# Performance work log

Measured on AMD Instinct MI355X. Metric: run time of the kernel, lower is better.

Reference implementation:

```python
import jax, jax.numpy as jnp
import numpy as np

B, T, S, D, H = 4, 1024, 1024, 1024, 16
DH = D // H  # head dim = 64
EPS = 1e-5
NEG = -1e9  # finite stand-in for -inf (grad-safe)


def setup_inputs() -> dict:
    key = jax.random.key(0)
    ks = jax.random.split(key, 9)
    std = D ** -0.5
    return {
        "q": jax.random.normal(ks[0], (B, T, D), jnp.float32),
        "k": jax.random.normal(ks[1], (B, S, D), jnp.float32),
        "v": jax.random.normal(ks[2], (B, S, D), jnp.float32),
        "attn_mask": jax.random.randint(ks[3], (T, S), 0, 2) == 1,
        "attn_bias": jax.random.normal(ks[4], (H, T, S), jnp.float32) * 0.1,
        "Wq": jax.random.normal(ks[5], (D, D), jnp.float32) * std,
        "Wk": jax.random.normal(ks[6], (D, D), jnp.float32) * std,
        "Wv": jax.random.normal(ks[7], (D, D), jnp.float32) * std,
        "Wo": jax.random.normal(ks[8], (D, D), jnp.float32) * std,
    }


def reference(q, k, v, attn_mask, attn_bias, Wq, Wk, Wv, Wo):
    # project and split heads: [B,T,D] -> [B,H,T,DH]
    qh = (q @ Wq.T).reshape(B, T, H, DH).transpose(0, 2, 1, 3) * (DH ** -0.5)
    kh = (k @ Wk.T).reshape(B, S, H, DH).transpose(0, 2, 1, 3)
    vh = (v @ Wv.T).reshape(B, S, H, DH).transpose(0, 2, 1, 3)
    # scores [B,H,T,S] with bias broadcast over batch, mask over (B,H)
    attn = jnp.einsum('bhtd,bhsd->bhts', qh, kh) + attn_bias
    attn = jnp.where(attn_mask, NEG, attn)
    # inverted softmax: normalize jointly over (heads, target) for each source pos
    a = jax.nn.softmax(attn.reshape(B, H * T, S), axis=1).reshape(B, H, T, S)
    a = jnp.where(attn_mask, 0.0, a)
    a = a / (a.sum(axis=-1, keepdims=True) + EPS)
    out = jnp.einsum('bhts,bhsd->bhtd', a, vh).transpose(0, 2, 1, 3).reshape(B, T, D)
    return out @ Wo.T
```

## Files before the change

kernel.cpp:

```cpp
#include <hip/hip_runtime.h>
#include <hip/hip_bf16.h>
#include <math.h>
#include <stdint.h>

#define B_ 4
#define T_ 1024
#define S_ 1024
#define D_ 1024
#define H_ 16
#define DH_ 64

static constexpr float EPSV = 1e-5f;
static constexpr float LOG2E = 1.4426950408889634f;
static constexpr float NEG2 = -1.4426950e9f;
static constexpr float SCALE_Q = 0.125f * LOG2E;

typedef __attribute__((ext_vector_type(8))) short short8;
typedef __attribute__((ext_vector_type(4))) float f32x4;

#define MFMA_BF16 __builtin_amdgcn_mfma_f32_16x16x32_bf16

__device__ __forceinline__ ushort f2bf(float f) {
  union { float f; unsigned u; } v; v.f = f;
  unsigned r = (v.u + 0x7FFFu + ((v.u >> 16) & 1u)) >> 16;
  return (ushort)r;
}
__device__ __forceinline__ float bf2f(ushort u) {
  union { unsigned u; float f; } v; v.u = (unsigned)u << 16;
  return v.f;
}
__device__ __forceinline__ float exp2_fast(float x) {
  float r;
  asm("v_exp_f32 %0, %1" : "=v"(r) : "v"(x));
  return r;
}
__device__ __forceinline__ unsigned cvt_pk_bf16(float lo, float hi) {
  unsigned r;
  asm("v_cvt_pk_bf16_f32 %0, %1, %2" : "=v"(r) : "v"(lo), "v"(hi));
  return r;
}

__device__ __forceinline__ void gl_lds16(const ushort* g, ushort* l) {
  __builtin_amdgcn_global_load_lds(
      (const __attribute__((address_space(1))) unsigned int*)g,
      (__attribute__((address_space(3))) unsigned int*)l, 16, 0, 0);
}

__global__ __launch_bounds__(256) void k_prep(
    const float* __restrict__ q, const float* __restrict__ k,
    const float* __restrict__ v, const float* __restrict__ Wq,
    const float* __restrict__ Wk, const float* __restrict__ Wv,
    const float* __restrict__ Wo, const float* __restrict__ bias,
    const int* __restrict__ mask, ushort* __restrict__ qb,
    ushort* __restrict__ kb, ushort* __restrict__ vb,
    ushort* __restrict__ Wqb, ushort* __restrict__ Wkb,
    ushort* __restrict__ Wvb, ushort* __restrict__ Wob,
    ushort* __restrict__ bm) {
  const int bid = blockIdx.x;
  if (bid < 12288) {
    const int which = bid >> 12, local = bid & 4095;
    const float* src = (which == 0) ? q : (which == 1) ? k : v;
    ushort* dst = (which == 0) ? qb : (which == 1) ? kb : vb;
    const int i = (local * 256 + threadIdx.x) * 4;
    float4 t = *(const float4*)(src + i);
    *(ushort4*)(dst + i) = make_ushort4(f2bf(t.x), f2bf(t.y), f2bf(t.z), f2bf(t.w));
  } else if (bid < 16384) {
    const int wv_ = bid - 12288;
    const int which = wv_ >> 10, local = wv_ & 1023;
    const float* src = (which == 0) ? Wq : (which == 1) ? Wk : (which == 2) ? Wv : Wo;
    ushort* dst = (which == 0) ? Wqb : (which == 1) ? Wkb : (which == 2) ? Wvb : Wob;
    const int i = (local * 256 + threadIdx.x) * 4;
    float4 t = *(const float4*)(src + i);
    *(ushort4*)(dst + i) = make_ushort4(f2bf(t.x), f2bf(t.y), f2bf(t.z), f2bf(t.w));
  } else {
    const size_t i = ((size_t)(bid - 16384) * 256 + threadIdx.x) * 8;
    const size_t mi = i & (size_t)(T_ * S_ - 1);
    float4 b0 = *(const float4*)(bias + i);
    float4 b1 = *(const float4*)(bias + i + 4);
    int4 m0 = *(const int4*)(mask + mi);
    int4 m1 = *(const int4*)(mask + mi + 4);
    ushort o[8];
    o[0] = f2bf(m0.x ? NEG2 : b0.x * LOG2E); o[1] = f2bf(m0.y ? NEG2 : b0.y * LOG2E);
    o[2] = f2bf(m0.z ? NEG2 : b0.z * LOG2E); o[3] = f2bf(m0.w ? NEG2 : b0.w * LOG2E);
    o[4] = f2bf(m1.x ? NEG2 : b1.x * LOG2E); o[5] = f2bf(m1.y ? NEG2 : b1.y * LOG2E);
    o[6] = f2bf(m1.z ? NEG2 : b1.z * LOG2E); o[7] = f2bf(m1.w ? NEG2 : b1.w * LOG2E);
    *(uint4*)(bm + i) = *(uint4*)o;
  }
}

template <int MODE>
__global__ __launch_bounds__(256) void k_gemm(const ushort* __restrict__ A,
                                              const ushort* __restrict__ W,
                                              void* __restrict__ Yv,
                                              float scale) {
  __shared__ ushort At[128][32];
  __shared__ ushort Wt[128][32];
  const int tid = threadIdx.x;
  const int l = tid & 63, w = tid >> 6;
  const int wm = (w >> 1) * 64, wn = (w & 1) * 64;
  const int r16 = l & 15, g = l >> 4;
  const int i0 = blockIdx.x * 128, j0 = blockIdx.y * 128;
  const int srow = (l >> 2), scol = (l & 3) << 3;
  f32x4 acc[4][4] = {};

  for (int k0 = 0; k0 < D_; k0 += 32) {
    __syncthreads();
#pragma unroll
    for (int u = 0; u < 2; ++u) {
      const int row = w * 32 + u * 16 + srow;
      gl_lds16(&A[(size_t)(i0 + row) * D_ + k0 + scol], &At[w * 32 + u * 16][0]);
      gl_lds16(&W[(size_t)(j0 + row) * D_ + k0 + scol], &Wt[w * 32 + u * 16][0]);
    }
    __syncthreads();
    short8 a0[4], b0[4];
#pragma unroll
    for (int i = 0; i < 4; ++i) a0[i] = *(const short8*)&At[wm + 16 * i + r16][g * 8];
#pragma unroll
    for (int j = 0; j < 4; ++j) b0[j] = *(const short8*)&Wt[wn + 16 * j + r16][g * 8];
#pragma unroll
    for (int i = 0; i < 4; ++i)
#pragma unroll
      for (int j = 0; j < 4; ++j)
        acc[i][j] = MFMA_BF16(a0[i], b0[j], acc[i][j], 0, 0, 0);
  }

#pragma unroll
  for (int i = 0; i < 4; ++i)
#pragma unroll
    for (int j = 0; j < 4; ++j) {
      if (MODE == 2) {
        const int row0 = i0 + wm + 16 * i + 4 * g;
        const int col = j0 + wn + 16 * j + r16;
        const int bb = row0 >> 10, s = row0 & 1023;
        const int hh = col >> 6, dh = col & 63;
        ushort4 pw;
        pw.x = f2bf(acc[i][j][0] * scale); pw.y = f2bf(acc[i][j][1] * scale);
        pw.z = f2bf(acc[i][j][2] * scale); pw.w = f2bf(acc[i][j][3] * scale);
        *(ushort4*)&((ushort*)Yv)[((size_t)(bb * H_ + hh) * DH_ + dh) * 1024 + s] = pw;
      } else {
#pragma unroll
        for (int r = 0; r < 4; ++r) {
          const int row = i0 + wm + 16 * i + 4 * g + r;
          const int col = j0 + wn + 16 * j + r16;
          const float vv = acc[i][j][r] * scale;
          if (MODE == 0) {
            ((float*)Yv)[(size_t)row * D_ + col] = vv;
          } else {
            const int b = row >> 10, t = row & 1023;
            const int h = col >> 6, dh = col & 63;
            ((ushort*)Yv)[(((size_t)(b * H_ + h) * 1024) + t) * DH_ + dh] = f2bf(vv);
          }
        }
      }
    }
}

__global__ __launch_bounds__(256, 4) void k_colstats(const ushort* __restrict__ Qh,
                                                     const ushort* __restrict__ Kh,
                                                     const ushort* __restrict__ biasm,
                                                     float* __restrict__ pc) {
  __shared__ ushort Qt[128][72];
  __shared__ ushort U[9216];
  ushort (*Kt)[72] = (ushort(*)[72])U;
  typedef ushort Row144[144];
  Row144* Bm0 = (Row144*)U;
  Row144* Bm1 = (Row144*)(U + 4608);

  const int z = blockIdx.z, b = z & 3, h = z >> 2;
  const int s0 = blockIdx.x * 128, t0 = blockIdx.y * 128;
  const int tid = threadIdx.x, l = tid & 63, w = tid >> 6;
  const int r16 = l & 15, g = l >> 4;

  const ushort* qsrc = Qh + ((size_t)((b * H_ + h) * 1024) + t0) * DH_;
  const ushort* ksrc = Kh + ((size_t)((b * H_ + h) * 1024) + s0) * DH_;
#pragma unroll
  for (int u = 0; u < 4; ++u) {
    const int lin = u * 256 + tid;
    const int row = lin >> 3, c8 = (lin & 7) << 3;
    *(uint4*)&Qt[row][c8] = *(const uint4*)&qsrc[(size_t)row * DH_ + c8];
    *(uint4*)&Kt[row][c8] = *(const uint4*)&ksrc[(size_t)row * DH_ + c8];
  }
  __syncthreads();

  f32x4 acc[8][2] = {};
#pragma unroll
  for (int kc = 0; kc < 2; ++kc) {
    short8 bk0 = *(const short8*)&Kt[w * 32 + r16][kc * 32 + g * 8];
    short8 bk1 = *(const short8*)&Kt[w * 32 + 16 + r16][kc * 32 + g * 8];
#pragma unroll
    for (int i = 0; i < 8; ++i) {
      short8 a = *(const short8*)&Qt[16 * i + r16][kc * 32 + g * 8];
      acc[i][0] = MFMA_BF16(a, bk0, acc[i][0], 0, 0, 0);
      acc[i][1] = MFMA_BF16(a, bk1, acc[i][1], 0, 0, 0);
    }
  }
  __syncthreads();

  const ushort* bsrc = biasm + ((size_t)h * 1024 + t0) * 1024 + s0;
#pragma unroll
  for (int u = 0; u < 2; ++u) {
    const int lin = u * 256 + tid;
    const int row = lin >> 4, c8 = (lin & 15) << 3;
    *(uint4*)&Bm0[row][c8] = *(const uint4*)&bsrc[(size_t)row * 1024 + c8];
  }
  __syncthreads();

  float cs0 = 0.f, cs1 = 0.f;
  const int col0 = w * 32 + r16;
#pragma unroll
  for (int c = 0; c < 4; ++c) {
    Row144* cur = (c & 1) ? Bm1 : Bm0;
    if (c < 3) {
      Row144* nxt = (c & 1) ? Bm0 : Bm1;
#pragma unroll
      for (int u = 0; u < 2; ++u) {
        const int lin = u * 256 + tid;
        const int row = lin >> 4, c8 = (lin & 15) << 3;
        *(uint4*)&nxt[row][c8] =
            *(const uint4*)&bsrc[(size_t)((c + 1) * 32 + row) * 1024 + c8];
      }
    }
#pragma unroll
    for (int ii = 0; ii < 2; ++ii) {
      const int i = 2 * c + ii;
      const int lrow = 16 * ii + 4 * g;
#pragma unroll
      for (int r = 0; r < 4; ++r) {
        cs0 += exp2_fast(acc[i][0][r] + bf2f(cur[lrow + r][col0]));
        cs1 += exp2_fast(acc[i][1][r] + bf2f(cur[lrow + r][col0 + 16]));
      }
    }
    __syncthreads();
  }

  cs0 += __shfl_xor(cs0, 16); cs0 += __shfl_xor(cs0, 32);
  cs1 += __shfl_xor(cs1, 16); cs1 += __shfl_xor(cs1, 32);
  if (g == 0) {
    const size_t base = ((size_t)b * 1024 + s0 + col0) * 128 + h * 8 + blockIdx.y;
    pc[base] = cs0;
    pc[base + 16 * 128] = cs1;
  }
}

__global__ __launch_bounds__(128) void k_combine(const float* __restrict__ pc,
                                                 float* __restrict__ Civ) {
  const int bs = blockIdx.x, tid = threadIdx.x;
  float c = pc[(size_t)bs * 128 + tid];
  __shared__ float sc[128];
  sc[tid] = c;
  __syncthreads();
  for (int off = 64; off > 0; off >>= 1) {
    if (tid < off) sc[tid] += sc[tid + off];
    __syncthreads();
  }
  if (tid == 0) {
    const float C = sc[0];
    Civ[bs] = (C > 0.f) ? 1.f / C : 0.f;
  }
}

__global__ __launch_bounds__(256, 3) void k_attn(const ushort* __restrict__ Qh,
                                                 const ushort* __restrict__ Kh,
                                                 const ushort* __restrict__ VhT,
                                                 const ushort* __restrict__ biasm,
                                                 const float* __restrict__ Civ,
                                                 ushort* __restrict__ O) {
  __shared__ ushort Kt[128][68];
  __shared__ ushort VtT[64][132];
  __shared__ ushort BmPt[64][132];
  __shared__ float Cih[128];
  __shared__ float Rp[4][64];

  const int bid = blockIdx.x;
  const int x8 = bid & 7;
  const int b = (bid >> 3) & 3;
  const int ht = (bid >> 5) * 8 + x8;
  const int h = ht >> 4, tt = ht & 15;
  const int t0 = tt * 64;
  const int bh = b * H_ + h;

  const int tid = threadIdx.x, l = tid & 63, w = tid >> 6;
  const int r16 = l & 15, g = l >> 4;
  const size_t kvbase = (size_t)bh * 1024 * DH_;
  const size_t vbase  = (size_t)bh * DH_ * 1024;

  short8 aq[4][2];
#pragma unroll
  for (int i = 0; i < 4; ++i) {
    const ushort* qr = Qh + ((size_t)bh * 1024 + t0 + 16 * i + r16) * DH_;
    aq[i][0] = *(const short8*)(qr + g * 8);
    aq[i][1] = *(const short8*)(qr + 32 + g * 8);
  }

  f32x4 aco[4] = {};
  float rloc[4] = {};

#pragma unroll 1
  for (int sc = 0; sc < 8; ++sc) {
    const int s0c = sc * 128;
    __syncthreads();

    {
      const ushort* ksrc = Kh + kvbase + (size_t)s0c * DH_;
#pragma unroll
      for (int u = 0; u < 4; ++u) {
        const int lin = u * 256 + tid;
        const int row = lin >> 3, c8 = (lin & 7) << 3;
        *(uint4*)&Kt[row][c8] = *(const uint4*)&ksrc[(size_t)row * DH_ + c8];
      }
      const ushort* vsrc = VhT + vbase + s0c;
      const ushort* bsrc = biasm + ((size_t)h * 1024 + t0) * 1024 + s0c;
#pragma unroll
      for (int u = 0; u < 4; ++u) {
        const int lin = u * 256 + tid;
        const int row = lin >> 4, c8 = (lin & 15) << 3;
        *(uint4*)&VtT[row][c8] = *(const uint4*)&vsrc[(size_t)row * 1024 + c8];
        *(uint4*)&BmPt[row][c8] = *(const uint4*)&bsrc[(size_t)row * 1024 + c8];
      }
      if (tid < 128) Cih[tid] = Civ[(size_t)b * 1024 + s0c + tid];
    }
    __syncthreads();

#pragma unroll
    for (int j2 = 0; j2 < 2; ++j2) {
      const int jf = 2 * w + j2;
      f32x4 as[4] = {};
      short8 kf0 = *(const short8*)&Kt[16 * jf + r16][g * 8];
      short8 kf1 = *(const short8*)&Kt[16 * jf + r16][32 + g * 8];
#pragma unroll
      for (int i = 0; i < 4; ++i) {
        as[i] = MFMA_BF16(kf0, aq[i][0], as[i], 0, 0, 0);
        as[i] = MFMA_BF16(kf1, aq[i][1], as[i], 0, 0, 0);
      }
      const int scol = 16 * jf + 4 * g;
      const float4 cv = *(const float4*)&Cih[scol];
#pragma unroll
      for (int i = 0; i < 4; ++i) {
        const int srow = 16 * i + r16;
        ushort4 bv4 = *(const ushort4*)&BmPt[srow][scol];
        const float p0 = exp2_fast(as[i][0] + bf2f(bv4.x)) * cv.x;
        const float p1 = exp2_fast(as[i][1] + bf2f(bv4.y)) * cv.y;
        const float p2 = exp2_fast(as[i][2] + bf2f(bv4.z)) * cv.z;
        const float p3 = exp2_fast(as[i][3] + bf2f(bv4.w)) * cv.w;
        rloc[i] += (p0 + p1) + (p2 + p3);
        uint2 pw;
        pw.x = cvt_pk_bf16(p0, p1);
        pw.y = cvt_pk_bf16(p2, p3);
        *(uint2*)&BmPt[srow][scol] = pw;
      }
    }
    __syncthreads();

#pragma unroll
    for (int kc = 0; kc < 4; ++kc) {
      short8 ap = *(const short8*)&BmPt[16 * w + r16][kc * 32 + g * 8];
#pragma unroll
      for (int j = 0; j < 4; ++j) {
        short8 bv = *(const short8*)&VtT[16 * j + r16][kc * 32 + g * 8];
        aco[j] = MFMA_BF16(ap, bv, aco[j], 0, 0, 0);
      }
    }
  }

#pragma unroll
  for (int i = 0; i < 4; ++i) {
    float vsum = rloc[i];
    vsum += __shfl_xor(vsum, 16);
    vsum += __shfl_xor(vsum, 32);
    if (l < 16) Rp[w][16 * i + r16] = vsum;
  }
  __syncthreads();

#pragma unroll
  for (int j = 0; j < 4; ++j)
#pragma unroll
    for (int r = 0; r < 4; ++r) {
      const int tl = 16 * w + 4 * g + r;
      const float R = Rp[0][tl] + Rp[1][tl] + Rp[2][tl] + Rp[3][tl];
      const float o = aco[j][r] / (R + EPSV);
      const int d = 16 * j + r16;
      O[((size_t)(b * 1024) + t0 + tl) * D_ + h * DH_ + d] = f2bf(o);
    }
}

extern "C" void kernel_launch(void* const* d_in, const int* in_sizes, int n_in,
                              void* d_out, int out_size, void* d_ws, size_t ws_size,
                              hipStream_t stream) {
  (void)in_sizes; (void)n_in; (void)out_size; (void)ws_size;
  const float* q    = (const float*)d_in[0];
  const float* k    = (const float*)d_in[1];
  const float* v    = (const float*)d_in[2];
  const int*   mask = (const int*)d_in[3];
  const float* bias = (const float*)d_in[4];
  const float* Wq   = (const float*)d_in[5];
  const float* Wk   = (const float*)d_in[6];
  const float* Wv   = (const float*)d_in[7];
  const float* Wo   = (const float*)d_in[8];
  float* out = (float*)d_out;

  ushort* qb   = (ushort*)d_ws;
  ushort* kb   = qb + 4194304;
  ushort* vb   = kb + 4194304;
  ushort* Wqb  = vb + 4194304;
  ushort* Wkb  = Wqb + 1048576;
  ushort* Wvb  = Wkb + 1048576;
  ushort* Wob  = Wvb + 1048576;
  ushort* Qh   = Wob + 1048576;
  ushort* Kh   = Qh + 4194304;
  ushort* VhT  = Kh + 4194304;
  ushort* Ob   = VhT + 4194304;
  ushort* bm   = Ob + 4194304;
  float*  pc   = (float*)(bm + 16777216);
  float*  Civ  = pc + 524288;

  k_prep<<<24576, 256, 0, stream>>>(q, k, v, Wq, Wk, Wv, Wo, bias, mask,
                                    qb, kb, vb, Wqb, Wkb, Wvb, Wob, bm);

  k_gemm<1><<<dim3(32, 8), 256, 0, stream>>>(qb, Wqb, Qh, SCALE_Q);
  k_gemm<1><<<dim3(32, 8), 256, 0, stream>>>(kb, Wkb, Kh, 1.0f);
  k_gemm<2><<<dim3(32, 8), 256, 0, stream>>>(vb, Wvb, VhT, 1.0f);

  k_colstats<<<dim3(8, 8, 64), 256, 0, stream>>>(Qh, Kh, bm, pc);
  k_combine<<<4096, 128, 0, stream>>>(pc, Civ);
  k_attn<<<1024, 256, 0, stream>>>(Qh, Kh, VhT, bm, Civ, Ob);

  k_gemm<0><<<dim3(32, 8), 256, 0, stream>>>(Ob, Wob, out, 1.0f);
}
```

Before: 196.1 us.

## Fuse fp32-to-bf16 input conversion into projection GEMMs and prefetch attention tiles

```diff
diff --git a/kernel.cpp b/kernel.cpp
--- a/kernel.cpp
+++ b/kernel.cpp
@@ -47,33 +47,22 @@
 }
 
 __global__ __launch_bounds__(256) void k_prep(
-    const float* __restrict__ q, const float* __restrict__ k,
-    const float* __restrict__ v, const float* __restrict__ Wq,
-    const float* __restrict__ Wk, const float* __restrict__ Wv,
-    const float* __restrict__ Wo, const float* __restrict__ bias,
-    const int* __restrict__ mask, ushort* __restrict__ qb,
-    ushort* __restrict__ kb, ushort* __restrict__ vb,
+    const float* __restrict__ Wq, const float* __restrict__ Wk,
+    const float* __restrict__ Wv, const float* __restrict__ Wo,
+    const float* __restrict__ bias, const int* __restrict__ mask,
     ushort* __restrict__ Wqb, ushort* __restrict__ Wkb,
     ushort* __restrict__ Wvb, ushort* __restrict__ Wob,
     ushort* __restrict__ bm) {
   const int bid = blockIdx.x;
-  if (bid < 12288) {
-    const int which = bid >> 12, local = bid & 4095;
-    const float* src = (which == 0) ? q : (which == 1) ? k : v;
-    ushort* dst = (which == 0) ? qb : (which == 1) ? kb : vb;
-    const int i = (local * 256 + threadIdx.x) * 4;
-    float4 t = *(const float4*)(src + i);
-    *(ushort4*)(dst + i) = make_ushort4(f2bf(t.x), f2bf(t.y), f2bf(t.z), f2bf(t.w));
-  } else if (bid < 16384) {
-    const int wv_ = bid - 12288;
-    const int which = wv_ >> 10, local = wv_ & 1023;
+  if (bid < 4096) {
+    const int which = bid >> 10, local = bid & 1023;
     const float* src = (which == 0) ? Wq : (which == 1) ? Wk : (which == 2) ? Wv : Wo;
     ushort* dst = (which == 0) ? Wqb : (which == 1) ? Wkb : (which == 2) ? Wvb : Wob;
     const int i = (local * 256 + threadIdx.x) * 4;
     float4 t = *(const float4*)(src + i);
     *(ushort4*)(dst + i) = make_ushort4(f2bf(t.x), f2bf(t.y), f2bf(t.z), f2bf(t.w));
   } else {
-    const size_t i = ((size_t)(bid - 16384) * 256 + threadIdx.x) * 8;
+    const size_t i = ((size_t)(bid - 4096) * 256 + threadIdx.x) * 8;
     const size_t mi = i & (size_t)(T_ * S_ - 1);
     float4 b0 = *(const float4*)(bias + i);
     float4 b1 = *(const float4*)(bias + i + 4);
@@ -88,12 +77,13 @@
   }
 }
 
-template <int MODE>
-__global__ __launch_bounds__(256) void k_gemm(const ushort* __restrict__ A,
+template <int MODE, bool AF32>
+__global__ __launch_bounds__(256) void k_gemm(const void* __restrict__ Av,
                                               const ushort* __restrict__ W,
                                               void* __restrict__ Yv,
                                               float scale) {
-  __shared__ ushort At[128][32];
+  constexpr int AST = AF32 ? 40 : 32;
+  __shared__ ushort At[128][AST];
   __shared__ ushort Wt[128][32];
   const int tid = threadIdx.x;
   const int l = tid & 63, w = tid >> 6;
@@ -108,8 +98,26 @@
 #pragma unroll
     for (int u = 0; u < 2; ++u) {
       const int row = w * 32 + u * 16 + srow;
-      gl_lds16(&A[(size_t)(i0 + row) * D_ + k0 + scol], &At[w * 32 + u * 16][0]);
       gl_lds16(&W[(size_t)(j0 + row) * D_ + k0 + scol], &Wt[w * 32 + u * 16][0]);
+      if (!AF32) {
+        gl_lds16(&((const ushort*)Av)[(size_t)(i0 + row) * D_ + k0 + scol],
+                 &At[w * 32 + u * 16][0]);
+      }
+    }
+    if (AF32) {
+      const float* A32 = (const float*)Av;
+#pragma unroll
+      for (int u = 0; u < 2; ++u) {
+        const int lin = u * 256 + tid;
+        const int row = lin >> 2, c8 = (lin & 3) << 3;
+        const float* src = &A32[(size_t)(i0 + row) * D_ + k0 + c8];
+        float4 f0 = *(const float4*)src;
+        float4 f1 = *(const float4*)(src + 4);
+        uint4 pk;
+        pk.x = cvt_pk_bf16(f0.x, f0.y); pk.y = cvt_pk_bf16(f0.z, f0.w);
+        pk.z = cvt_pk_bf16(f1.x, f1.y); pk.w = cvt_pk_bf16(f1.z, f1.w);
+        *(uint4*)&At[row][c8] = pk;
+      }
     }
     __syncthreads();
     short8 a0[4], b0[4];
@@ -284,6 +292,9 @@
   const size_t kvbase = (size_t)bh * 1024 * DH_;
   const size_t vbase  = (size_t)bh * DH_ * 1024;
 
+  const int krow = tid >> 1, kc8 = (tid & 1) << 5;
+  (void)krow; (void)kc8;
+
   short8 aq[4][2];
 #pragma unroll
   for (int i = 0; i < 4; ++i) {
@@ -295,31 +306,48 @@
   f32x4 aco[4] = {};
   float rloc[4] = {};
 
+  uint4 skr[4], svr[4], sbr[4];
+  float civreg = 0.f;
+
+  {
+    const ushort* ksrc = Kh + kvbase;
+    const ushort* vsrc = VhT + vbase;
+    const ushort* bsrc = biasm + ((size_t)h * 1024 + t0) * 1024;
+#pragma unroll
+    for (int u = 0; u < 4; ++u) {
+      const int lin = u * 256 + tid;
+      skr[u] = *(const uint4*)&ksrc[(size_t)(lin >> 3) * DH_ + ((lin & 7) << 3)];
+      svr[u] = *(const uint4*)&vsrc[(size_t)(lin >> 4) * 1024 + ((lin & 15) << 3)];
+      sbr[u] = *(const uint4*)&bsrc[(size_t)(lin >> 4) * 1024 + ((lin & 15) << 3)];
+    }
+    if (tid < 128) civreg = Civ[(size_t)b * 1024 + tid];
+  }
+#pragma unroll
+  for (int u = 0; u < 4; ++u) {
+    const int lin = u * 256 + tid;
+    *(uint4*)&Kt[lin >> 3][(lin & 7) << 3] = skr[u];
+    *(uint4*)&VtT[lin >> 4][(lin & 15) << 3] = svr[u];
+    *(uint4*)&BmPt[lin >> 4][(lin & 15) << 3] = sbr[u];
+  }
+  if (tid < 128) Cih[tid] = civreg;
+  __syncthreads();
+
 #pragma unroll 1
   for (int sc = 0; sc < 8; ++sc) {
-    const int s0c = sc * 128;
-    __syncthreads();
-
-    {
-      const ushort* ksrc = Kh + kvbase + (size_t)s0c * DH_;
+    if (sc < 7) {
+      const int s0n = (sc + 1) * 128;
+      const ushort* ksrc = Kh + kvbase + (size_t)s0n * DH_;
+      const ushort* vsrc = VhT + vbase + s0n;
+      const ushort* bsrc = biasm + ((size_t)h * 1024 + t0) * 1024 + s0n;
 #pragma unroll
       for (int u = 0; u < 4; ++u) {
         const int lin = u * 256 + tid;
-        const int row = lin >> 3, c8 = (lin & 7) << 3;
-        *(uint4*)&Kt[row][c8] = *(const uint4*)&ksrc[(size_t)row * DH_ + c8];
-      }
-      const ushort* vsrc = VhT + vbase + s0c;
-      const ushort* bsrc = biasm + ((size_t)h * 1024 + t0) * 1024 + s0c;
-#pragma unroll
-      for (int u = 0; u < 4; ++u) {
-        const int lin = u * 256 + tid;
-        const int row = lin >> 4, c8 = (lin & 15) << 3;
-        *(uint4*)&VtT[row][c8] = *(const uint4*)&vsrc[(size_t)row * 1024 + c8];
-        *(uint4*)&BmPt[row][c8] = *(const uint4*)&bsrc[(size_t)row * 1024 + c8];
-      }
-      if (tid < 128) Cih[tid] = Civ[(size_t)b * 1024 + s0c + tid];
-    }
-    __syncthreads();
+        skr[u] = *(const uint4*)&ksrc[(size_t)(lin >> 3) * DH_ + ((lin & 7) << 3)];
+        svr[u] = *(const uint4*)&vsrc[(size_t)(lin >> 4) * 1024 + ((lin & 15) << 3)];
+        sbr[u] = *(const uint4*)&bsrc[(size_t)(lin >> 4) * 1024 + ((lin & 15) << 3)];
+      }
+      if (tid < 128) civreg = Civ[(size_t)b * 1024 + s0n + tid];
+    }
 
 #pragma unroll
     for (int j2 = 0; j2 < 2; ++j2) {
@@ -359,6 +387,19 @@
         short8 bv = *(const short8*)&VtT[16 * j + r16][kc * 32 + g * 8];
         aco[j] = MFMA_BF16(ap, bv, aco[j], 0, 0, 0);
       }
+    }
+    __syncthreads();
+
+    if (sc < 7) {
+#pragma unroll
+      for (int u = 0; u < 4; ++u) {
+        const int lin = u * 256 + tid;
+        *(uint4*)&Kt[lin >> 3][(lin & 7) << 3] = skr[u];
+        *(uint4*)&VtT[lin >> 4][(lin & 15) << 3] = svr[u];
+        *(uint4*)&BmPt[lin >> 4][(lin & 15) << 3] = sbr[u];
+      }
+      if (tid < 128) Cih[tid] = civreg;
+      __syncthreads();
     }
   }
 
@@ -398,10 +439,7 @@
   const float* Wo   = (const float*)d_in[8];
   float* out = (float*)d_out;
 
-  ushort* qb   = (ushort*)d_ws;
-  ushort* kb   = qb + 4194304;
-  ushort* vb   = kb + 4194304;
-  ushort* Wqb  = vb + 4194304;
+  ushort* Wqb  = (ushort*)d_ws;
   ushort* Wkb  = Wqb + 1048576;
   ushort* Wvb  = Wkb + 1048576;
   ushort* Wob  = Wvb + 1048576;
@@ -413,16 +451,16 @@
   float*  pc   = (float*)(bm + 16777216);
   float*  Civ  = pc + 524288;
 
-  k_prep<<<24576, 256, 0, stream>>>(q, k, v, Wq, Wk, Wv, Wo, bias, mask,
-                                    qb, kb, vb, Wqb, Wkb, Wvb, Wob, bm);
-
-  k_gemm<1><<<dim3(32, 8), 256, 0, stream>>>(qb, Wqb, Qh, SCALE_Q);
-  k_gemm<1><<<dim3(32, 8), 256, 0, stream>>>(kb, Wkb, Kh, 1.0f);
-  k_gemm<2><<<dim3(32, 8), 256, 0, stream>>>(vb, Wvb, VhT, 1.0f);
+  k_prep<<<12288, 256, 0, stream>>>(Wq, Wk, Wv, Wo, bias, mask,
+                                    Wqb, Wkb, Wvb, Wob, bm);
+
+  k_gemm<1, true><<<dim3(32, 8), 256, 0, stream>>>(q, Wqb, Qh, SCALE_Q);
+  k_gemm<1, true><<<dim3(32, 8), 256, 0, stream>>>(k, Wkb, Kh, 1.0f);
+  k_gemm<2, true><<<dim3(32, 8), 256, 0, stream>>>(v, Wvb, VhT, 1.0f);
 
   k_colstats<<<dim3(8, 8, 64), 256, 0, stream>>>(Qh, Kh, bm, pc);
   k_combine<<<4096, 128, 0, stream>>>(pc, Civ);
   k_attn<<<1024, 256, 0, stream>>>(Qh, Kh, VhT, bm, Civ, Ob);
 
-  k_gemm<0><<<dim3(32, 8), 256, 0, stream>>>(Ob, Wob, out, 1.0f);
-}
+  k_gemm<0, false><<<dim3(32, 8), 256, 0, stream>>>(Ob, Wob, out, 1.0f);
+}
```

After: 344.8 us. 1.76x slower.

## Restructure column-stats kernel to stream K tiles per 64-row Q block

Applied to the files above, without the earlier changes.

```diff
diff --git a/kernel.cpp b/kernel.cpp
--- a/kernel.cpp
+++ b/kernel.cpp
@@ -158,105 +158,98 @@
 __global__ __launch_bounds__(256, 4) void k_colstats(const ushort* __restrict__ Qh,
                                                      const ushort* __restrict__ Kh,
                                                      const ushort* __restrict__ biasm,
-                                                     float* __restrict__ pc) {
-  __shared__ ushort Qt[128][72];
-  __shared__ ushort U[9216];
-  ushort (*Kt)[72] = (ushort(*)[72])U;
-  typedef ushort Row144[144];
-  Row144* Bm0 = (Row144*)U;
-  Row144* Bm1 = (Row144*)(U + 4608);
-
-  const int z = blockIdx.z, b = z & 3, h = z >> 2;
-  const int s0 = blockIdx.x * 128, t0 = blockIdx.y * 128;
+                                                     float* __restrict__ pcT) {
+  __shared__ ushort Kt[128][68];
+  __shared__ ushort Bm[64][132];
+
+  const int bid = blockIdx.x;
+  const int x8 = bid & 7;
+  const int b = (bid >> 3) & 3;
+  const int ht = (bid >> 5) * 8 + x8;
+  const int h = ht >> 4, tt = ht & 15;
+  const int t0 = tt * 64;
+  const int bh = b * H_ + h;
+
   const int tid = threadIdx.x, l = tid & 63, w = tid >> 6;
   const int r16 = l & 15, g = l >> 4;
-
-  const ushort* qsrc = Qh + ((size_t)((b * H_ + h) * 1024) + t0) * DH_;
-  const ushort* ksrc = Kh + ((size_t)((b * H_ + h) * 1024) + s0) * DH_;
-#pragma unroll
-  for (int u = 0; u < 4; ++u) {
-    const int lin = u * 256 + tid;
-    const int row = lin >> 3, c8 = (lin & 7) << 3;
-    *(uint4*)&Qt[row][c8] = *(const uint4*)&qsrc[(size_t)row * DH_ + c8];
-    *(uint4*)&Kt[row][c8] = *(const uint4*)&ksrc[(size_t)row * DH_ + c8];
-  }
-  __syncthreads();
-
-  f32x4 acc[8][2] = {};
-#pragma unroll
-  for (int kc = 0; kc < 2; ++kc) {
-    short8 bk0 = *(const short8*)&Kt[w * 32 + r16][kc * 32 + g * 8];
-    short8 bk1 = *(const short8*)&Kt[w * 32 + 16 + r16][kc * 32 + g * 8];
-#pragma unroll
-    for (int i = 0; i < 8; ++i) {
-      short8 a = *(const short8*)&Qt[16 * i + r16][kc * 32 + g * 8];
-      acc[i][0] = MFMA_BF16(a, bk0, acc[i][0], 0, 0, 0);
-      acc[i][1] = MFMA_BF16(a, bk1, acc[i][1], 0, 0, 0);
-    }
-  }
-  __syncthreads();
-
-  const ushort* bsrc = biasm + ((size_t)h * 1024 + t0) * 1024 + s0;
-#pragma unroll
-  for (int u = 0; u < 2; ++u) {
-    const int lin = u * 256 + tid;
-    const int row = lin >> 4, c8 = (lin & 15) << 3;
-    *(uint4*)&Bm0[row][c8] = *(const uint4*)&bsrc[(size_t)row * 1024 + c8];
-  }
-  __syncthreads();
-
-  float cs0 = 0.f, cs1 = 0.f;
-  const int col0 = w * 32 + r16;
-#pragma unroll
-  for (int c = 0; c < 4; ++c) {
-    Row144* cur = (c & 1) ? Bm1 : Bm0;
-    if (c < 3) {
-      Row144* nxt = (c & 1) ? Bm0 : Bm1;
-#pragma unroll
-      for (int u = 0; u < 2; ++u) {
+  const size_t kvbase = (size_t)bh * 1024 * DH_;
+
+  short8 aq[4][2];
+#pragma unroll
+  for (int i = 0; i < 4; ++i) {
+    const ushort* qr = Qh + ((size_t)bh * 1024 + t0 + 16 * i + r16) * DH_;
+    aq[i][0] = *(const short8*)(qr + g * 8);
+    aq[i][1] = *(const short8*)(qr + 32 + g * 8);
+  }
+
+  float* pbase = pcT + (size_t)(h * 16 + tt) * 4096 + (size_t)b * 1024;
+
+#pragma unroll 1
+  for (int sc = 0; sc < 8; ++sc) {
+    const int s0c = sc * 128;
+    __syncthreads();
+    {
+      const ushort* ksrc = Kh + kvbase + (size_t)s0c * DH_;
+#pragma unroll
+      for (int u = 0; u < 4; ++u) {
+        const int lin = u * 256 + tid;
+        const int row = lin >> 3, c8 = (lin & 7) << 3;
+        *(uint4*)&Kt[row][c8] = *(const uint4*)&ksrc[(size_t)row * DH_ + c8];
+      }
+      const ushort* bsrc = biasm + ((size_t)h * 1024 + t0) * 1024 + s0c;
+#pragma unroll
+      for (int u = 0; u < 4; ++u) {
         const int lin = u * 256 + tid;
         const int row = lin >> 4, c8 = (lin & 15) << 3;
-        *(uint4*)&nxt[row][c8] =
-            *(const uint4*)&bsrc[(size_t)((c + 1) * 32 + row) * 1024 + c8];
-      }
-    }
-#pragma unroll
-    for (int ii = 0; ii < 2; ++ii) {
-      const int i = 2 * c + ii;
-      const int lrow = 16 * ii + 4 * g;
-#pragma unroll
-      for (int r = 0; r < 4; ++r) {
-        cs0 += exp2_fast(acc[i][0][r] + bf2f(cur[lrow + r][col0]));
-        cs1 += exp2_fast(acc[i][1][r] + bf2f(cur[lrow + r][col0 + 16]));
-      }
-    }
-    __syncthreads();
-  }
-
-  cs0 += __shfl_xor(cs0, 16); cs0 += __shfl_xor(cs0, 32);
-  cs1 += __shfl_xor(cs1, 16); cs1 += __shfl_xor(cs1, 32);
-  if (g == 0) {
-    const size_t base = ((size_t)b * 1024 + s0 + col0) * 128 + h * 8 + blockIdx.y;
-    pc[base] = cs0;
-    pc[base + 16 * 128] = cs1;
-  }
-}
-
-__global__ __launch_bounds__(128) void k_combine(const float* __restrict__ pc,
+        *(uint4*)&Bm[row][c8] = *(const uint4*)&bsrc[(size_t)row * 1024 + c8];
+      }
+    }
+    __syncthreads();
+
+#pragma unroll
+    for (int j2 = 0; j2 < 2; ++j2) {
+      const int jf = 2 * w + j2;
+      f32x4 as[4] = {};
+      short8 kf0 = *(const short8*)&Kt[16 * jf + r16][g * 8];
+      short8 kf1 = *(const short8*)&Kt[16 * jf + r16][32 + g * 8];
+#pragma unroll
+      for (int i = 0; i < 4; ++i) {
+        as[i] = MFMA_BF16(kf0, aq[i][0], as[i], 0, 0, 0);
+        as[i] = MFMA_BF16(kf1, aq[i][1], as[i], 0, 0, 0);
+      }
+      const int scol = 16 * jf + 4 * g;
+      float cs0 = 0.f, cs1 = 0.f, cs2 = 0.f, cs3 = 0.f;
+#pragma unroll
+      for (int i = 0; i < 4; ++i) {
+        const int srow = 16 * i + r16;
+        ushort4 bv4 = *(const ushort4*)&Bm[srow][scol];
+        cs0 += exp2_fast(as[i][0] + bf2f(bv4.x));
+        cs1 += exp2_fast(as[i][1] + bf2f(bv4.y));
+        cs2 += exp2_fast(as[i][2] + bf2f(bv4.z));
+        cs3 += exp2_fast(as[i][3] + bf2f(bv4.w));
+      }
+#pragma unroll
+      for (int m = 1; m < 16; m <<= 1) {
+        cs0 += __shfl_xor(cs0, m);
+        cs1 += __shfl_xor(cs1, m);
+        cs2 += __shfl_xor(cs2, m);
+        cs3 += __shfl_xor(cs3, m);
+      }
+      if (r16 == 0) {
+        float4 o = make_float4(cs0, cs1, cs2, cs3);
+        *(float4*)&pbase[s0c + scol] = o;
+      }
+    }
+  }
+}
+
+__global__ __launch_bounds__(256) void k_combine(const float* __restrict__ pcT,
                                                  float* __restrict__ Civ) {
-  const int bs = blockIdx.x, tid = threadIdx.x;
-  float c = pc[(size_t)bs * 128 + tid];
-  __shared__ float sc[128];
-  sc[tid] = c;
-  __syncthreads();
-  for (int off = 64; off > 0; off >>= 1) {
-    if (tid < off) sc[tid] += sc[tid + off];
-    __syncthreads();
-  }
-  if (tid == 0) {
-    const float C = sc[0];
-    Civ[bs] = (C > 0.f) ? 1.f / C : 0.f;
-  }
+  const int i = blockIdx.x * 256 + threadIdx.x;
+  float s = 0.f;
+#pragma unroll 4
+  for (int p = 0; p < 256; ++p) s += pcT[(size_t)p * 4096 + i];
+  Civ[i] = (s > 0.f) ? 1.f / s : 0.f;
 }
 
 __global__ __launch_bounds__(256, 3) void k_attn(const ushort* __restrict__ Qh,
@@ -410,8 +403,8 @@
   ushort* VhT  = Kh + 4194304;
   ushort* Ob   = VhT + 4194304;
   ushort* bm   = Ob + 4194304;
-  float*  pc   = (float*)(bm + 16777216);
-  float*  Civ  = pc + 524288;
+  float*  pcT  = (float*)(bm + 16777216);
+  float*  Civ  = pcT + 1048576;
 
   k_prep<<<24576, 256, 0, stream>>>(q, k, v, Wq, Wk, Wv, Wo, bias, mask,
                                     qb, kb, vb, Wqb, Wkb, Wvb, Wob, bm);
@@ -420,8 +413,8 @@
   k_gemm<1><<<dim3(32, 8), 256, 0, stream>>>(kb, Wkb, Kh, 1.0f);
   k_gemm<2><<<dim3(32, 8), 256, 0, stream>>>(vb, Wvb, VhT, 1.0f);
 
-  k_colstats<<<dim3(8, 8, 64), 256, 0, stream>>>(Qh, Kh, bm, pc);
-  k_combine<<<4096, 128, 0, stream>>>(pc, Civ);
+  k_colstats<<<1024, 256, 0, stream>>>(Qh, Kh, bm, pcT);
+  k_combine<<<16, 256, 0, stream>>>(pcT, Civ);
   k_attn<<<1024, 256, 0, stream>>>(Qh, Kh, VhT, bm, Civ, Ob);
 
   k_gemm<0><<<dim3(32, 8), 256, 0, stream>>>(Ob, Wob, out, 1.0f);
```

Result: slower. 218.0 us (+11.1%).
